# Performance work log

Measured on AMD Instinct MI355X. Metric: run time of the kernel, lower is better.

The kernel has to match this reference:

```python
import jax, jax.numpy as jnp
import numpy as np

K, D = 2048, 256
B, H, W = 16, 64, 64
DECAY = 0.99
EPS = 1e-05


def setup_inputs() -> dict:
    key = jax.random.key(0)
    k1, k2, k3 = jax.random.split(key, 3)
    z_e = jax.random.normal(k1, (B, D, H, W), dtype=jnp.float32)
    codebook = jax.random.normal(k2, (K, D), dtype=jnp.float32)
    ema_count = jnp.zeros((K,), dtype=jnp.float32)
    ema_weight = jax.random.normal(k3, (K, D), dtype=jnp.float32)
    return {"z_e": z_e, "codebook": codebook, "ema_count": ema_count, "ema_weight": ema_weight}


def reference(z_e, codebook, ema_count, ema_weight):
    b, d, h, w = z_e.shape
    k = codebook.shape[0]
    # [B, D, H, W] -> [B*H*W, D]
    flat = jnp.transpose(z_e, (0, 2, 3, 1)).reshape(-1, d)
    # squared euclidean distances to each code: [N, K]
    dist = (jnp.sum(flat * flat, axis=1, keepdims=True)
            - 2.0 * (flat @ codebook.T)
            + jnp.sum(codebook * codebook, axis=1))
    idx = jnp.argmin(dist, axis=1)  # [N] int
    # gather nearest codes -> [B, D, H, W]
    z_q = jnp.transpose(codebook[idx].reshape(b, h, w, d), (0, 3, 1, 2))
    # EMA statistics (training path, no_grad in torch)
    n = jax.ops.segment_sum(jnp.ones_like(idx, dtype=flat.dtype), idx, num_segments=k)  # [K]
    dw = jax.ops.segment_sum(flat, idx, num_segments=k)  # [K, D]
    new_ema_count = ema_count * DECAY + (1.0 - DECAY) * n
    new_ema_weight = ema_weight * DECAY + (1.0 - DECAY) * dw
    new_codebook = new_ema_weight / (new_ema_count + EPS)[:, None]
    # commitment loss and straight-through estimator
    loss_commit = jnp.mean(jnp.square(z_e - z_q))
    z_q_st = z_e + jax.lax.stop_gradient(z_q - z_e)
    return (z_q_st, idx.reshape(b, h, w), loss_commit,
            new_codebook, new_ema_count, new_ema_weight)
```

## Files before the change

kernel.cpp:

```cpp
#include <hip/hip_runtime.h>
#include <hip/hip_bf16.h>


#define KC 2048
#define DD 256
#define NB 16
#define HWS 4096
#define NPTS 65536
#define DECAYF 0.99f
#define ONEMD 0.01f
#define EPSF 1e-5f
#define NCH 2
#define MARGIN 0.0625f
#define CHPTS 32
#define FPT 64
#define NLOSS 4096

typedef __attribute__((ext_vector_type(8))) short short8v;
typedef __attribute__((ext_vector_type(16))) float f32x16;

#define WS_IDX     0
#define WS_SORTED  262144
#define WS_CNTI    524288
#define WS_START   532480
#define WS_CURSOR  540672
#define WS_FLAGCNT 548864
#define WS_FLAGS   549120
#define WS_LOSSP   549120
#define WS_CNORM   811264
#define WS_PART    819456
#define WS_CBH     5013760
#define WS_CBL     6062336
#define WS_ZH      7110912
#define WS_ZL      40665344
#define WS_NEED_MFMA 74219776ULL
#define WS_NEED_MID  5013760ULL

#define OUT_ZQ   0
#define OUT_IDX  16777216
#define OUT_LOSS (OUT_IDX + NPTS)
#define OUT_CB   (OUT_LOSS + 1)
#define OUT_CNT  (OUT_CB + KC*DD)
#define OUT_W    (OUT_CNT + KC)

static __device__ __forceinline__ unsigned short f2bf_rn(float x) {
    unsigned u = __builtin_bit_cast(unsigned, x);
    unsigned r = (u + 0x7FFFu + ((u >> 16) & 1u)) >> 16;
    return (unsigned short)r;
}
static __device__ __forceinline__ float bf2f(unsigned short h) {
    unsigned u = ((unsigned)h) << 16;
    return __builtin_bit_cast(float, u);
}
static __device__ __forceinline__ void gload_lds16(const unsigned short* g,
                                                   unsigned short* l) {
    __builtin_amdgcn_global_load_lds(
        (const __attribute__((address_space(1))) void*)g,
        (__attribute__((address_space(3))) void*)l, 16, 0, 0);
}

__global__ __launch_bounds__(256) void prep_kernel(const float* __restrict__ z_e,
                                                   const float* __restrict__ cb,
                                                   float* __restrict__ cnorm,
                                                   unsigned short* __restrict__ cbs_h,
                                                   unsigned short* __restrict__ cbs_l,
                                                   unsigned short* __restrict__ zh,
                                                   unsigned short* __restrict__ zl,
                                                   int* __restrict__ cnti,
                                                   int* __restrict__ flagcnt) {
    const int tid = threadIdx.x;
    if (blockIdx.x >= 4096) {
        int k = (blockIdx.x - 4096) * 256 + tid;
        cnti[k] = 0;
        if (k == 0) *flagcnt = 0;
        const int ct = k >> 5, lc = k & 31;
        const float4* row = reinterpret_cast<const float4*>(cb + (size_t)k * DD);
        float s = 0.f;
        #pragma unroll 4
        for (int chunk = 0; chunk < 32; ++chunk) {
            float4 v0 = row[chunk * 2], v1 = row[chunk * 2 + 1];
            float v[8] = {v0.x, v0.y, v0.z, v0.w, v1.x, v1.y, v1.z, v1.w};
            unsigned short hh[8], ll[8];
            #pragma unroll
            for (int j = 0; j < 8; ++j) {
                s += v[j] * v[j];
                hh[j] = f2bf_rn(v[j]);
                ll[j] = f2bf_rn(v[j] - bf2f(hh[j]));
            }
            const int ks = chunk >> 1, h = chunk & 1;
            size_t dst = (size_t)ct * 8192 + ks * 512 + (h * 32 + lc) * 8;
            *reinterpret_cast<ushort4*>(cbs_h + dst)     = *(ushort4*)&hh[0];
            *reinterpret_cast<ushort4*>(cbs_h + dst + 4) = *(ushort4*)&hh[4];
            *reinterpret_cast<ushort4*>(cbs_l + dst)     = *(ushort4*)&ll[0];
            *reinterpret_cast<ushort4*>(cbs_l + dst + 4) = *(ushort4*)&ll[4];
        }
        cnorm[k] = s;
        return;
    }
    __shared__ float t_lds[64][65];
    const int bid = blockIdx.x;
    const int hw0 = (bid & 63) * 64;
    const int d0 = ((bid >> 6) & 3) * 64;
    const int b = bid >> 8;
    const float* src = z_e + (size_t)b * DD * HWS;
    #pragma unroll
    for (int i = 0; i < 16; ++i) {
        int li = tid + i * 256;
        int d = li >> 6, hw = li & 63;
        t_lds[d][hw] = src[(size_t)(d0 + d) * HWS + hw0 + hw];
    }
    __syncthreads();
    #pragma unroll
    for (int i = 0; i < 16; ++i) {
        int li = tid + i * 256;
        int p = li >> 6, d = li & 63;
        float x = t_lds[d][p];
        unsigned short h = f2bf_rn(x);
        unsigned short l = f2bf_rn(x - bf2f(h));
        size_t o = ((size_t)b * HWS + hw0 + p) * DD + d0 + d;
        zh[o] = h; zl[o] = l;
    }
}

__global__ __launch_bounds__(256) void cnorm_kernel(const float* __restrict__ cb,
                                                    float* __restrict__ cnorm) {
    int k = blockIdx.x * 256 + threadIdx.x;
    if (k < KC) {
        const float4* row = reinterpret_cast<const float4*>(cb + (size_t)k * DD);
        float s = 0.f;
        #pragma unroll 8
        for (int i = 0; i < DD / 4; ++i) {
            float4 v = row[i];
            s += v.x * v.x + v.y * v.y + v.z * v.z + v.w * v.w;
        }
        cnorm[k] = s;
    }
}

__global__ __launch_bounds__(256, 2) void argmin_mfma_kernel(const unsigned short* __restrict__ zh,
                                                             const unsigned short* __restrict__ zl,
                                                             const unsigned short* __restrict__ cbs_h,
                                                             const unsigned short* __restrict__ cbs_l,
                                                             const float* __restrict__ cnorm,
                                                             int* __restrict__ idx_out,
                                                             int* __restrict__ cnti,
                                                             int* __restrict__ flagcnt,
                                                             int* __restrict__ flaglist,
                                                             unsigned long long* __restrict__ fixmin) {
    __shared__ unsigned short lds_cb[2][2][16][512];

    const int tid = threadIdx.x;
    const int w = tid >> 6, lane = tid & 63;
    const int lc = lane & 31, h = lane >> 5;
    const int p = blockIdx.x * 128 + w * 32 + lc;

    const short8v* zhp = reinterpret_cast<const short8v*>(zh + (size_t)p * DD + h * 8);
    const short8v* zlp = reinterpret_cast<const short8v*>(zl + (size_t)p * DD + h * 8);
    short8v bh[16], bl[16];
    #pragma unroll
    for (int ks = 0; ks < 16; ++ks) { bh[ks] = zhp[ks * 2]; bl[ks] = zlp[ks * 2]; }

    auto stage = [&](int ct, int buf) {
        #pragma unroll
        for (int j = 0; j < 8; ++j) {
            const int inst = w * 8 + j;
            const int part = inst >> 4;
            const int ks = inst & 15;
            const unsigned short* src =
                (part ? cbs_l : cbs_h) + (size_t)ct * 8192 + ks * 512 + lane * 8;
            gload_lds16(src, &lds_cb[buf][part][ks][0]);
        }
    };

    float bv1 = 3.4e38f, bv2 = 3.4e38f;
    int bi1 = 0;
    int cur = 0;

    stage(0, 0);
    __syncthreads();

    for (int ct = 0; ct < KC / 32; ++ct) {
        if (ct + 1 < KC / 32) stage(ct + 1, cur ^ 1);

        f32x16 a0, a1, a2;
        #pragma unroll
        for (int i = 0; i < 16; ++i) { a0[i] = 0.f; a1[i] = 0.f; a2[i] = 0.f; }
        #pragma unroll
        for (int ks = 0; ks < 16; ++ks) {
            short8v ah = *reinterpret_cast<const short8v*>(&lds_cb[cur][0][ks][lane * 8]);
            short8v al = *reinterpret_cast<const short8v*>(&lds_cb[cur][1][ks][lane * 8]);
            a0 = __builtin_amdgcn_mfma_f32_32x32x16_bf16(ah, bh[ks], a0, 0, 0, 0);
            a1 = __builtin_amdgcn_mfma_f32_32x32x16_bf16(ah, bl[ks], a1, 0, 0, 0);
            a2 = __builtin_amdgcn_mfma_f32_32x32x16_bf16(al, bh[ks], a2, 0, 0, 0);
        }
        const float* cnb = cnorm + ct * 32 + h * 4;
        #pragma unroll
        for (int g = 0; g < 4; ++g) {
            float4 cn = *reinterpret_cast<const float4*>(cnb + g * 8);
            float cna[4] = {cn.x, cn.y, cn.z, cn.w};
            #pragma unroll
            for (int q = 0; q < 4; ++q) {
                float dot = a0[g * 4 + q] + a1[g * 4 + q] + a2[g * 4 + q];
                float v = fmaf(dot, -2.0f, cna[q]);
                int k = ct * 32 + g * 8 + h * 4 + q;
                bool lt = v < bv1;
                bv2 = fminf(bv2, fmaxf(v, bv1));
                bv1 = fminf(bv1, v);
                bi1 = lt ? k : bi1;
            }
        }
        __syncthreads();
        cur ^= 1;
    }

    float ov1 = __shfl_xor(bv1, 32, 64);
    float ov2 = __shfl_xor(bv2, 32, 64);
    int   oi1 = __shfl_xor(bi1, 32, 64);
    float nv1 = fminf(bv1, ov1);
    float nv2 = fminf(fmaxf(bv1, ov1), fminf(bv2, ov2));
    int ni1 = (ov1 < bv1 || (ov1 == bv1 && oi1 < bi1)) ? oi1 : bi1;

    if (h == 0) {
        idx_out[p] = ni1;
        atomicAdd(&cnti[ni1], 1);
        if (nv2 - nv1 < MARGIN) {
            int pos = atomicAdd(flagcnt, 1);
            flaglist[pos] = p;
            fixmin[pos] = ~0ULL;
        }
    }
}

__global__ __launch_bounds__(256) void fixup_part_kernel(const float* __restrict__ z_e,
                                                         const float* __restrict__ cb,
                                                         const float* __restrict__ cnorm,
                                                         const int* __restrict__ flagcnt,
                                                         const int* __restrict__ flaglist,
                                                         unsigned long long* __restrict__ fixmin) {
    __shared__ float As[64][FPT + 4];
    __shared__ float Bs[64][64 + 4];
    __shared__ float rv[FPT][16];
    __shared__ int   ri[FPT][16];
    __shared__ int   zo[FPT];

    const int tid = threadIdx.x;
    const int tx = tid & 15, ty = tid >> 4;
    const int tot = *flagcnt;
    const int base = blockIdx.x * FPT;
    if (base >= tot) return;
    const int cnt = min(FPT, tot - base);
    const int kt = blockIdx.y * 64;

    if (tid < FPT) {
        int n = flaglist[base + ((tid < cnt) ? tid : 0)];
        zo[tid] = (n >> 12) * DD * HWS + (n & 4095);
    }
    __syncthreads();

    float acc[4][4] = {};
    for (int dc = 0; dc < DD; dc += 64) {
        #pragma unroll
        for (int i = 0; i < 16; ++i) {
            int li = tid + i * 256;
            int d = li >> 6, pp = li & 63;
            As[d][pp] = z_e[(size_t)zo[pp] + (size_t)(dc + d) * HWS];
        }
        #pragma unroll
        for (int i = 0; i < 16; ++i) {
            int li = tid + i * 256;
            int k = li >> 6, d = li & 63;
            Bs[d][k] = cb[(size_t)(kt + k) * DD + dc + d];
        }
        __syncthreads();
        #pragma unroll
        for (int d = 0; d < 64; ++d) {
            const float4 a4 = *reinterpret_cast<const float4*>(&As[d][ty * 4]);
            const float4 b4 = *reinterpret_cast<const float4*>(&Bs[d][tx * 4]);
            const float a[4] = {a4.x, a4.y, a4.z, a4.w};
            const float bb[4] = {b4.x, b4.y, b4.z, b4.w};
            #pragma unroll
            for (int j = 0; j < 4; ++j)
                #pragma unroll
                for (int i = 0; i < 4; ++i)
                    acc[j][i] = fmaf(a[j], bb[i], acc[j][i]);
        }
        __syncthreads();
    }

    float bestv[4]; int besti[4];
    #pragma unroll
    for (int j = 0; j < 4; ++j) { bestv[j] = 3.4e38f; besti[j] = 0; }
    #pragma unroll
    for (int i = 0; i < 4; ++i) {
        int k = kt + tx * 4 + i;
        float c = cnorm[k];
        #pragma unroll
        for (int j = 0; j < 4; ++j) {
            float dist = c - 2.0f * acc[j][i];
            if (dist < bestv[j]) { bestv[j] = dist; besti[j] = k; }
        }
    }
    #pragma unroll
    for (int j = 0; j < 4; ++j) { rv[ty * 4 + j][tx] = bestv[j]; ri[ty * 4 + j][tx] = besti[j]; }
    __syncthreads();

    if (tid < cnt) {
        float bv = rv[tid][0]; int bi = ri[tid][0];
        #pragma unroll
        for (int t = 1; t < 16; ++t) {
            float v = rv[tid][t]; int i2 = ri[tid][t];
            if (v < bv || (v == bv && i2 < bi)) { bv = v; bi = i2; }
        }
        unsigned uv = __float_as_uint(bv);
        uv = (uv & 0x80000000u) ? ~uv : (uv | 0x80000000u);
        unsigned long long key = ((unsigned long long)uv << 32) | (unsigned)bi;
        atomicMin(&fixmin[base + tid], key);
    }
}

__global__ __launch_bounds__(256) void fixup_apply_kernel(const int* __restrict__ flagcnt,
                                                          const int* __restrict__ flaglist,
                                                          const unsigned long long* __restrict__ fixmin,
                                                          int* __restrict__ idx_out,
                                                          int* __restrict__ cnti) {
    int f = blockIdx.x * 256 + threadIdx.x;
    if (f < *flagcnt) {
        int n = flaglist[f];
        int nk = (int)(fixmin[f] & 0xFFFFFFFFull);
        int ok = idx_out[n];
        if (nk != ok) {
            atomicSub(&cnti[ok], 1);
            atomicAdd(&cnti[nk], 1);
            idx_out[n] = nk;
        }
    }
}

#define PT 64
#define KT 64
#define DC 64
__global__ __launch_bounds__(256) void argmin_kernel(const float* __restrict__ z_e,
                                                     const float* __restrict__ cb,
                                                     const float* __restrict__ cnorm,
                                                     int* __restrict__ idx_out) {
    __shared__ float As[DC][PT + 4];
    __shared__ float Bs[DC][KT + 4];
    __shared__ float rv[PT][16];
    __shared__ int   ri[PT][16];
    const int tid = threadIdx.x;
    const int tx = tid & 15, ty = tid >> 4;
    const int n0 = blockIdx.x * PT;
    const int b = n0 >> 12;
    const int hw0 = n0 & 4095;
    const float* zb = z_e + (size_t)b * DD * HWS + hw0;
    float bestv[4]; int besti[4];
    #pragma unroll
    for (int j = 0; j < 4; ++j) { bestv[j] = 3.4e38f; besti[j] = 0; }
    for (int kt = 0; kt < KC; kt += KT) {
        float acc[4][4] = {};
        for (int dc = 0; dc < DD; dc += DC) {
            #pragma unroll
            for (int i = 0; i < 16; ++i) {
                int li = tid + i * 256;
                int d = li >> 6, pp = li & 63;
                As[d][pp] = zb[(size_t)(dc + d) * HWS + pp];
            }
            #pragma unroll
            for (int i = 0; i < 16; ++i) {
                int li = tid + i * 256;
                int k = li >> 6, d = li & 63;
                Bs[d][k] = cb[(size_t)(kt + k) * DD + dc + d];
            }
            __syncthreads();
            #pragma unroll
            for (int d = 0; d < DC; ++d) {
                const float4 a4 = *reinterpret_cast<const float4*>(&As[d][ty * 4]);
                const float4 b4 = *reinterpret_cast<const float4*>(&Bs[d][tx * 4]);
                const float a[4] = {a4.x, a4.y, a4.z, a4.w};
                const float bb[4] = {b4.x, b4.y, b4.z, b4.w};
                #pragma unroll
                for (int j = 0; j < 4; ++j)
                    #pragma unroll
                    for (int i = 0; i < 4; ++i)
                        acc[j][i] = fmaf(a[j], bb[i], acc[j][i]);
            }
            __syncthreads();
        }
        #pragma unroll
        for (int i = 0; i < 4; ++i) {
            int k = kt + tx * 4 + i;
            float c = cnorm[k];
            #pragma unroll
            for (int j = 0; j < 4; ++j) {
                float dist = c - 2.0f * acc[j][i];
                if (dist < bestv[j]) { bestv[j] = dist; besti[j] = k; }
            }
        }
    }
    #pragma unroll
    for (int j = 0; j < 4; ++j) { rv[ty * 4 + j][tx] = bestv[j]; ri[ty * 4 + j][tx] = besti[j]; }
    __syncthreads();
    if (tid < PT) {
        float bv = rv[tid][0]; int bi = ri[tid][0];
        #pragma unroll
        for (int t = 1; t < 16; ++t) {
            float v = rv[tid][t]; int i2 = ri[tid][t];
            if (v < bv || (v == bv && i2 < bi)) { bv = v; bi = i2; }
        }
        idx_out[n0 + tid] = bi;
    }
}

__global__ __launch_bounds__(256) void hist_kernel(const int* __restrict__ idx,
                                                   int* __restrict__ cnti) {
    int n = blockIdx.x * 256 + threadIdx.x;
    atomicAdd(&cnti[idx[n]], 1);
}

__global__ __launch_bounds__(256) void scan_kernel(const int* __restrict__ cnt,
                                                   int* __restrict__ start,
                                                   int* __restrict__ cursor) {
    __shared__ int ps[256];
    const int t = threadIdx.x;
    int v[8], s = 0;
    #pragma unroll
    for (int j = 0; j < 8; ++j) { v[j] = cnt[t * 8 + j]; s += v[j]; }
    ps[t] = s;
    __syncthreads();
    for (int off = 1; off < 256; off <<= 1) {
        int x = (t >= off) ? ps[t - off] : 0;
        __syncthreads();
        ps[t] += x;
        __syncthreads();
    }
    int base = ps[t] - s;
    #pragma unroll
    for (int j = 0; j < 8; ++j) { start[t * 8 + j] = base; cursor[t * 8 + j] = base; base += v[j]; }
}

__global__ __launch_bounds__(256) void scatter_ids_kernel(const int* __restrict__ idx,
                                                          int* __restrict__ cursor,
                                                          int* __restrict__ sorted,
                                                          float* __restrict__ out_idxf,
                                                          float* __restrict__ dwacc) {
    int n = blockIdx.x * 256 + threadIdx.x;
    int k = idx[n];
    out_idxf[n] = (float)k;
    int pos = atomicAdd(&cursor[k], 1);
    sorted[pos] = n;
    #pragma unroll
    for (int i = 0; i < (KC * DD) / NPTS; ++i)
        dwacc[n + i * NPTS] = 0.f;
}

__global__ __launch_bounds__(256) void dw_chunk_kernel(const unsigned short* __restrict__ zh,
                                                       const unsigned short* __restrict__ zl,
                                                       const int* __restrict__ sorted,
                                                       const int* __restrict__ idx,
                                                       float* __restrict__ dwacc) {
    const int t = threadIdx.x;
    const int base = blockIdx.x * CHPTS;
    int kcur = idx[sorted[base]];
    float acc = 0.f;
    for (int i = 0; i < CHPTS; ++i) {
        const int n = sorted[base + i];
        const int k = idx[n];
        if (k != kcur) {
            atomicAdd(&dwacc[(size_t)kcur * DD + t], acc);
            acc = 0.f; kcur = k;
        }
        acc += bf2f(zh[(size_t)n * DD + t]) + bf2f(zl[(size_t)n * DD + t]);
    }
    atomicAdd(&dwacc[(size_t)kcur * DD + t], acc);
}

__global__ __launch_bounds__(256) void dw_direct_kernel(const float* __restrict__ z_e,
                                                        const int* __restrict__ sorted,
                                                        const int* __restrict__ start,
                                                        const int* __restrict__ cnti,
                                                        float* __restrict__ part) {
    const int k = blockIdx.x, c = blockIdx.y, t = threadIdx.x;
    const int s0 = start[k], cnt = cnti[k];
    float acc = 0.f;
    for (int p = c; p < cnt; p += NCH) {
        int n = sorted[s0 + p];
        int b = n >> 12, hw = n & 4095;
        acc += z_e[(size_t)b * DD * HWS + (size_t)t * HWS + hw];
    }
    part[((size_t)k * NCH + c) * DD + t] = acc;
}

__global__ __launch_bounds__(256) void zq_loss_kernel(const float* __restrict__ z_e,
                                                      const float* __restrict__ cb,
                                                      const int* __restrict__ idx,
                                                      float* __restrict__ out_zq,
                                                      float* __restrict__ lossp) {
    const int tid = threadIdx.x;
    const size_t base = ((size_t)blockIdx.x * 256 + tid) * 16;
    const int hw = (int)(base & 4095);
    const int d = (int)((base >> 12) & 255);
    const int b = (int)(base >> 20);
    const int n0 = b * HWS + hw;

    const int4* ip = reinterpret_cast<const int4*>(idx + n0);
    const float4* zp = reinterpret_cast<const float4*>(z_e + base);
    float4* op = reinterpret_cast<float4*>(out_zq + base);

    float ls = 0.f;
    #pragma unroll
    for (int g = 0; g < 4; ++g) {
        int4 i4 = ip[g];
        float4 z4 = zp[g];
        int kk[4] = {i4.x, i4.y, i4.z, i4.w};
        float zz[4] = {z4.x, z4.y, z4.z, z4.w};
        float o4[4];
        #pragma unroll
        for (int q = 0; q < 4; ++q) {
            float qv = cb[(size_t)kk[q] * DD + d];
            o4[q] = zz[q] + (qv - zz[q]);
            float df = zz[q] - qv;
            ls += df * df;
        }
        float4 w4; w4.x = o4[0]; w4.y = o4[1]; w4.z = o4[2]; w4.w = o4[3];
        op[g] = w4;
    }

    #pragma unroll
    for (int off = 32; off > 0; off >>= 1) ls += __shfl_down(ls, off, 64);
    __shared__ float wsum[4];
    if ((tid & 63) == 0) wsum[tid >> 6] = ls;
    __syncthreads();
    if (tid == 0) lossp[blockIdx.x] = wsum[0] + wsum[1] + wsum[2] + wsum[3];
}

__global__ __launch_bounds__(256) void finalize_dw_kernel(const float* __restrict__ ema_count,
                                                          const float* __restrict__ ema_weight,
                                                          const int* __restrict__ cnti,
                                                          const float* __restrict__ dwacc,
                                                          const float* __restrict__ lossp,
                                                          float* __restrict__ out_cb,
                                                          float* __restrict__ out_cnt,
                                                          float* __restrict__ out_w,
                                                          float* __restrict__ out_loss) {
    const int t = blockIdx.x * 256 + threadIdx.x;
    const int k = t >> 8, d = t & 255;
    const float nc = ema_count[k] * DECAYF + ONEMD * (float)cnti[k];
    const float nw = ema_weight[t] * DECAYF + ONEMD * dwacc[t];
    out_w[t] = nw;
    out_cb[t] = nw / (nc + EPSF);
    if (d == 0) out_cnt[k] = nc;

    if (blockIdx.x == 0) {
        __shared__ double sd[256];
        const int tid = threadIdx.x;
        double s = 0.0;
        for (int i = tid; i < NLOSS; i += 256) s += (double)lossp[i];
        sd[tid] = s;
        __syncthreads();
        for (int off = 128; off > 0; off >>= 1) {
            if (tid < off) sd[tid] += sd[tid + off];
            __syncthreads();
        }
        if (tid == 0) out_loss[0] = (float)(sd[0] / 16777216.0);
    }
}

__global__ __launch_bounds__(256) void finalize_part_kernel(const float* __restrict__ ema_count,
                                                            const float* __restrict__ ema_weight,
                                                            const int* __restrict__ cnti,
                                                            const float* __restrict__ part,
                                                            const float* __restrict__ lossp,
                                                            float* __restrict__ out_cb,
                                                            float* __restrict__ out_cnt,
                                                            float* __restrict__ out_w,
                                                            float* __restrict__ out_loss) {
    const int t = blockIdx.x * 256 + threadIdx.x;
    const int k = t >> 8, d = t & 255;
    float dw = 0.f;
    #pragma unroll
    for (int c = 0; c < NCH; ++c) dw += part[((size_t)k * NCH + c) * DD + d];
    const float nc = ema_count[k] * DECAYF + ONEMD * (float)cnti[k];
    const float nw = ema_weight[t] * DECAYF + ONEMD * dw;
    out_w[t] = nw;
    out_cb[t] = nw / (nc + EPSF);
    if (d == 0) out_cnt[k] = nc;

    if (blockIdx.x == 0) {
        __shared__ double sd[256];
        const int tid = threadIdx.x;
        double s = 0.0;
        for (int i = tid; i < NLOSS; i += 256) s += (double)lossp[i];
        sd[tid] = s;
        __syncthreads();
        for (int off = 128; off > 0; off >>= 1) {
            if (tid < off) sd[tid] += sd[tid + off];
            __syncthreads();
        }
        if (tid == 0) out_loss[0] = (float)(sd[0] / 16777216.0);
    }
}

extern "C" void kernel_launch(void* const* d_in, const int* in_sizes, int n_in,
                              void* d_out, int out_size, void* d_ws, size_t ws_size,
                              hipStream_t stream) {
    const float* z_e       = (const float*)d_in[0];
    const float* codebook  = (const float*)d_in[1];
    const float* ema_count = (const float*)d_in[2];
    const float* ema_weight= (const float*)d_in[3];
    float* out = (float*)d_out;
    char* ws = (char*)d_ws;

    int*   ws_idx    = (int*)(ws + WS_IDX);
    int*   ws_sorted = (int*)(ws + WS_SORTED);
    int*   ws_cnti   = (int*)(ws + WS_CNTI);
    int*   ws_start  = (int*)(ws + WS_START);
    int*   ws_cursor = (int*)(ws + WS_CURSOR);
    int*   ws_flagc  = (int*)(ws + WS_FLAGCNT);
    int*   ws_flags  = (int*)(ws + WS_FLAGS);
    float* ws_lossp  = (float*)(ws + WS_LOSSP);
    float* ws_cnorm  = (float*)(ws + WS_CNORM);
    unsigned long long* ws_fixmin = (unsigned long long*)(ws + WS_PART);
    float* ws_dwacc  = (float*)(ws + WS_PART);
    float* ws_part   = (float*)(ws + WS_PART);
    unsigned short* ws_cbh = (unsigned short*)(ws + WS_CBH);
    unsigned short* ws_cbl = (unsigned short*)(ws + WS_CBL);
    unsigned short* ws_zh  = (unsigned short*)(ws + WS_ZH);
    unsigned short* ws_zl  = (unsigned short*)(ws + WS_ZL);

    const bool mfma_path = (ws_size >= WS_NEED_MFMA);
    const bool mid_path  = (ws_size >= WS_NEED_MID);

    if (mfma_path) {
        prep_kernel<<<4104, 256, 0, stream>>>(z_e, codebook, ws_cnorm, ws_cbh, ws_cbl,
                                              ws_zh, ws_zl, ws_cnti, ws_flagc);
        argmin_mfma_kernel<<<NPTS / 128, 256, 0, stream>>>(ws_zh, ws_zl, ws_cbh, ws_cbl,
                                                           ws_cnorm, ws_idx, ws_cnti,
                                                           ws_flagc, ws_flags, ws_fixmin);
        fixup_part_kernel<<<dim3(NPTS / FPT, KC / 64), 256, 0, stream>>>(z_e, codebook, ws_cnorm,
                                                                         ws_flagc, ws_flags,
                                                                         ws_fixmin);
        fixup_apply_kernel<<<NPTS / 256, 256, 0, stream>>>(ws_flagc, ws_flags, ws_fixmin,
                                                           ws_idx, ws_cnti);
        zq_loss_kernel<<<NLOSS, 256, 0, stream>>>(z_e, codebook, ws_idx,
                                                  out + OUT_ZQ, ws_lossp);
        scan_kernel<<<1, 256, 0, stream>>>(ws_cnti, ws_start, ws_cursor);
        scatter_ids_kernel<<<NPTS / 256, 256, 0, stream>>>(ws_idx, ws_cursor, ws_sorted,
                                                           out + OUT_IDX, ws_dwacc);
        dw_chunk_kernel<<<NPTS / CHPTS, 256, 0, stream>>>(ws_zh, ws_zl, ws_sorted,
                                                          ws_idx, ws_dwacc);
        finalize_dw_kernel<<<(KC * DD) / 256, 256, 0, stream>>>(ema_count, ema_weight,
                                                                ws_cnti, ws_dwacc, ws_lossp,
                                                                out + OUT_CB, out + OUT_CNT,
                                                                out + OUT_W, out + OUT_LOSS);
    } else if (mid_path) {
        hipMemsetAsync(ws + WS_CNTI, 0, (size_t)(WS_FLAGCNT + 256 - WS_CNTI), stream);
        cnorm_kernel<<<(KC + 255) / 256, 256, 0, stream>>>(codebook, ws_cnorm);
        argmin_kernel<<<NPTS / PT, 256, 0, stream>>>(z_e, codebook, ws_cnorm, ws_idx);
        zq_loss_kernel<<<NLOSS, 256, 0, stream>>>(z_e, codebook, ws_idx,
                                                  out + OUT_ZQ, ws_lossp);
        hist_kernel<<<NPTS / 256, 256, 0, stream>>>(ws_idx, ws_cnti);
        scan_kernel<<<1, 256, 0, stream>>>(ws_cnti, ws_start, ws_cursor);
        scatter_ids_kernel<<<NPTS / 256, 256, 0, stream>>>(ws_idx, ws_cursor, ws_sorted,
                                                           out + OUT_IDX, ws_part);
        dw_direct_kernel<<<dim3(KC, NCH), 256, 0, stream>>>(z_e, ws_sorted,
                                                            ws_start, ws_cnti, ws_part + KC * DD);
        finalize_part_kernel<<<(KC * DD) / 256, 256, 0, stream>>>(ema_count, ema_weight,
                                                                  ws_cnti, ws_part + KC * DD,
                                                                  ws_lossp,
                                                                  out + OUT_CB, out + OUT_CNT,
                                                                  out + OUT_W, out + OUT_LOSS);
    }
}
```

Measured before the change: 409.3 us.

## Double per-wave point tile in MFMA argmin and fuse tail kernels

```diff
diff --git a/kernel.cpp b/kernel.cpp
--- a/kernel.cpp
+++ b/kernel.cpp
@@ -137,7 +137,7 @@
     }
 }
 
-__global__ __launch_bounds__(256, 2) void argmin_mfma_kernel(const unsigned short* __restrict__ zh,
+__global__ __launch_bounds__(256, 1) void argmin_mfma_kernel(const unsigned short* __restrict__ zh,
                                                              const unsigned short* __restrict__ zl,
                                                              const unsigned short* __restrict__ cbs_h,
                                                              const unsigned short* __restrict__ cbs_l,
@@ -152,13 +152,19 @@
     const int tid = threadIdx.x;
     const int w = tid >> 6, lane = tid & 63;
     const int lc = lane & 31, h = lane >> 5;
-    const int p = blockIdx.x * 128 + w * 32 + lc;
-
-    const short8v* zhp = reinterpret_cast<const short8v*>(zh + (size_t)p * DD + h * 8);
-    const short8v* zlp = reinterpret_cast<const short8v*>(zl + (size_t)p * DD + h * 8);
-    short8v bh[16], bl[16];
-    #pragma unroll
-    for (int ks = 0; ks < 16; ++ks) { bh[ks] = zhp[ks * 2]; bl[ks] = zlp[ks * 2]; }
+    const int p0 = blockIdx.x * 256 + w * 64 + lc;
+    const int p1 = p0 + 32;
+
+    const short8v* zhp0 = reinterpret_cast<const short8v*>(zh + (size_t)p0 * DD + h * 8);
+    const short8v* zlp0 = reinterpret_cast<const short8v*>(zl + (size_t)p0 * DD + h * 8);
+    const short8v* zhp1 = reinterpret_cast<const short8v*>(zh + (size_t)p1 * DD + h * 8);
+    const short8v* zlp1 = reinterpret_cast<const short8v*>(zl + (size_t)p1 * DD + h * 8);
+    short8v bh0[16], bl0[16], bh1[16], bl1[16];
+    #pragma unroll
+    for (int ks = 0; ks < 16; ++ks) {
+        bh0[ks] = zhp0[ks * 2]; bl0[ks] = zlp0[ks * 2];
+        bh1[ks] = zhp1[ks * 2]; bl1[ks] = zlp1[ks * 2];
+    }
 
     auto stage = [&](int ct, int buf) {
         #pragma unroll
@@ -172,8 +178,9 @@
         }
     };
 
-    float bv1 = 3.4e38f, bv2 = 3.4e38f;
-    int bi1 = 0;
+    float bv1_0 = 3.4e38f, bv2_0 = 3.4e38f;
+    float bv1_1 = 3.4e38f, bv2_1 = 3.4e38f;
+    int bi1_0 = 0, bi1_1 = 0;
     int cur = 0;
 
     stage(0, 0);
@@ -182,16 +189,22 @@
     for (int ct = 0; ct < KC / 32; ++ct) {
         if (ct + 1 < KC / 32) stage(ct + 1, cur ^ 1);
 
-        f32x16 a0, a1, a2;
-        #pragma unroll
-        for (int i = 0; i < 16; ++i) { a0[i] = 0.f; a1[i] = 0.f; a2[i] = 0.f; }
+        f32x16 a0, a1, a2, c0, c1, c2;
+        #pragma unroll
+        for (int i = 0; i < 16; ++i) {
+            a0[i] = 0.f; a1[i] = 0.f; a2[i] = 0.f;
+            c0[i] = 0.f; c1[i] = 0.f; c2[i] = 0.f;
+        }
         #pragma unroll
         for (int ks = 0; ks < 16; ++ks) {
             short8v ah = *reinterpret_cast<const short8v*>(&lds_cb[cur][0][ks][lane * 8]);
             short8v al = *reinterpret_cast<const short8v*>(&lds_cb[cur][1][ks][lane * 8]);
-            a0 = __builtin_amdgcn_mfma_f32_32x32x16_bf16(ah, bh[ks], a0, 0, 0, 0);
-            a1 = __builtin_amdgcn_mfma_f32_32x32x16_bf16(ah, bl[ks], a1, 0, 0, 0);
-            a2 = __builtin_amdgcn_mfma_f32_32x32x16_bf16(al, bh[ks], a2, 0, 0, 0);
+            a0 = __builtin_amdgcn_mfma_f32_32x32x16_bf16(ah, bh0[ks], a0, 0, 0, 0);
+            c0 = __builtin_amdgcn_mfma_f32_32x32x16_bf16(ah, bh1[ks], c0, 0, 0, 0);
+            a1 = __builtin_amdgcn_mfma_f32_32x32x16_bf16(ah, bl0[ks], a1, 0, 0, 0);
+            c1 = __builtin_amdgcn_mfma_f32_32x32x16_bf16(ah, bl1[ks], c1, 0, 0, 0);
+            a2 = __builtin_amdgcn_mfma_f32_32x32x16_bf16(al, bh0[ks], a2, 0, 0, 0);
+            c2 = __builtin_amdgcn_mfma_f32_32x32x16_bf16(al, bh1[ks], c2, 0, 0, 0);
         }
         const float* cnb = cnorm + ct * 32 + h * 4;
         #pragma unroll
@@ -200,33 +213,57 @@
             float cna[4] = {cn.x, cn.y, cn.z, cn.w};
             #pragma unroll
             for (int q = 0; q < 4; ++q) {
-                float dot = a0[g * 4 + q] + a1[g * 4 + q] + a2[g * 4 + q];
-                float v = fmaf(dot, -2.0f, cna[q]);
                 int k = ct * 32 + g * 8 + h * 4 + q;
-                bool lt = v < bv1;
-                bv2 = fminf(bv2, fmaxf(v, bv1));
-                bv1 = fminf(bv1, v);
-                bi1 = lt ? k : bi1;
+                float dot0 = a0[g * 4 + q] + a1[g * 4 + q] + a2[g * 4 + q];
+                float v0 = fmaf(dot0, -2.0f, cna[q]);
+                bool lt0 = v0 < bv1_0;
+                bv2_0 = fminf(bv2_0, fmaxf(v0, bv1_0));
+                bv1_0 = fminf(bv1_0, v0);
+                bi1_0 = lt0 ? k : bi1_0;
+                float dot1 = c0[g * 4 + q] + c1[g * 4 + q] + c2[g * 4 + q];
+                float v1 = fmaf(dot1, -2.0f, cna[q]);
+                bool lt1 = v1 < bv1_1;
+                bv2_1 = fminf(bv2_1, fmaxf(v1, bv1_1));
+                bv1_1 = fminf(bv1_1, v1);
+                bi1_1 = lt1 ? k : bi1_1;
             }
         }
         __syncthreads();
         cur ^= 1;
     }
 
-    float ov1 = __shfl_xor(bv1, 32, 64);
-    float ov2 = __shfl_xor(bv2, 32, 64);
-    int   oi1 = __shfl_xor(bi1, 32, 64);
-    float nv1 = fminf(bv1, ov1);
-    float nv2 = fminf(fmaxf(bv1, ov1), fminf(bv2, ov2));
-    int ni1 = (ov1 < bv1 || (ov1 == bv1 && oi1 < bi1)) ? oi1 : bi1;
-
-    if (h == 0) {
-        idx_out[p] = ni1;
-        atomicAdd(&cnti[ni1], 1);
-        if (nv2 - nv1 < MARGIN) {
-            int pos = atomicAdd(flagcnt, 1);
-            flaglist[pos] = p;
-            fixmin[pos] = ~0ULL;
+    {
+        float ov1 = __shfl_xor(bv1_0, 32, 64);
+        float ov2 = __shfl_xor(bv2_0, 32, 64);
+        int   oi1 = __shfl_xor(bi1_0, 32, 64);
+        float nv1 = fminf(bv1_0, ov1);
+        float nv2 = fminf(fmaxf(bv1_0, ov1), fminf(bv2_0, ov2));
+        int ni1 = (ov1 < bv1_0 || (ov1 == bv1_0 && oi1 < bi1_0)) ? oi1 : bi1_0;
+        if (h == 0) {
+            idx_out[p0] = ni1;
+            atomicAdd(&cnti[ni1], 1);
+            if (nv2 - nv1 < MARGIN) {
+                int pos = atomicAdd(flagcnt, 1);
+                flaglist[pos] = p0;
+                fixmin[pos] = ~0ULL;
+            }
+        }
+    }
+    {
+        float ov1 = __shfl_xor(bv1_1, 32, 64);
+        float ov2 = __shfl_xor(bv2_1, 32, 64);
+        int   oi1 = __shfl_xor(bi1_1, 32, 64);
+        float nv1 = fminf(bv1_1, ov1);
+        float nv2 = fminf(fmaxf(bv1_1, ov1), fminf(bv2_1, ov2));
+        int ni1 = (ov1 < bv1_1 || (ov1 == bv1_1 && oi1 < bi1_1)) ? oi1 : bi1_1;
+        if (h == 0) {
+            idx_out[p1] = ni1;
+            atomicAdd(&cnti[ni1], 1);
+            if (nv2 - nv1 < MARGIN) {
+                int pos = atomicAdd(flagcnt, 1);
+                flaglist[pos] = p1;
+                fixmin[pos] = ~0ULL;
+            }
         }
     }
 }
@@ -246,85 +283,90 @@
     const int tid = threadIdx.x;
     const int tx = tid & 15, ty = tid >> 4;
     const int tot = *flagcnt;
-    const int base = blockIdx.x * FPT;
-    if (base >= tot) return;
-    const int cnt = min(FPT, tot - base);
     const int kt = blockIdx.y * 64;
 
-    if (tid < FPT) {
-        int n = flaglist[base + ((tid < cnt) ? tid : 0)];
-        zo[tid] = (n >> 12) * DD * HWS + (n & 4095);
-    }
-    __syncthreads();
-
-    float acc[4][4] = {};
-    for (int dc = 0; dc < DD; dc += 64) {
-        #pragma unroll
-        for (int i = 0; i < 16; ++i) {
-            int li = tid + i * 256;
-            int d = li >> 6, pp = li & 63;
-            As[d][pp] = z_e[(size_t)zo[pp] + (size_t)(dc + d) * HWS];
-        }
-        #pragma unroll
-        for (int i = 0; i < 16; ++i) {
-            int li = tid + i * 256;
-            int k = li >> 6, d = li & 63;
-            Bs[d][k] = cb[(size_t)(kt + k) * DD + dc + d];
-        }
+    for (int cbk = blockIdx.x; cbk * FPT < tot; cbk += gridDim.x) {
+        const int base = cbk * FPT;
+        const int cnt = min(FPT, tot - base);
         __syncthreads();
-        #pragma unroll
-        for (int d = 0; d < 64; ++d) {
-            const float4 a4 = *reinterpret_cast<const float4*>(&As[d][ty * 4]);
-            const float4 b4 = *reinterpret_cast<const float4*>(&Bs[d][tx * 4]);
-            const float a[4] = {a4.x, a4.y, a4.z, a4.w};
-            const float bb[4] = {b4.x, b4.y, b4.z, b4.w};
-            #pragma unroll
-            for (int j = 0; j < 4; ++j)
+        if (tid < FPT) {
+            int n = flaglist[base + ((tid < cnt) ? tid : 0)];
+            zo[tid] = (n >> 12) * DD * HWS + (n & 4095);
+        }
+        __syncthreads();
+
+        float acc[4][4] = {};
+        for (int dc = 0; dc < DD; dc += 64) {
+            #pragma unroll
+            for (int i = 0; i < 16; ++i) {
+                int li = tid + i * 256;
+                int d = li >> 6, pp = li & 63;
+                As[d][pp] = z_e[(size_t)zo[pp] + (size_t)(dc + d) * HWS];
+            }
+            #pragma unroll
+            for (int i = 0; i < 16; ++i) {
+                int li = tid + i * 256;
+                int k = li >> 6, d = li & 63;
+                Bs[d][k] = cb[(size_t)(kt + k) * DD + dc + d];
+            }
+            __syncthreads();
+            #pragma unroll
+            for (int d = 0; d < 64; ++d) {
+                const float4 a4 = *reinterpret_cast<const float4*>(&As[d][ty * 4]);
+                const float4 b4 = *reinterpret_cast<const float4*>(&Bs[d][tx * 4]);
+                const float a[4] = {a4.x, a4.y, a4.z, a4.w};
+                const float bb[4] = {b4.x, b4.y, b4.z, b4.w};
                 #pragma unroll
-                for (int i = 0; i < 4; ++i)
-                    acc[j][i] = fmaf(a[j], bb[i], acc[j][i]);
-        }
+                for (int j = 0; j < 4; ++j)
+                    #pragma unroll
+                    for (int i = 0; i < 4; ++i)
+                        acc[j][i] = fmaf(a[j], bb[i], acc[j][i]);
+            }
+            __syncthreads();
+        }
+
+        float bestv[4]; int besti[4];
+        #pragma unroll
+        for (int j = 0; j < 4; ++j) { bestv[j] = 3.4e38f; besti[j] = 0; }
+        #pragma unroll
+        for (int i = 0; i < 4; ++i) {
+            int k = kt + tx * 4 + i;
+            float c = cnorm[k];
+            #pragma unroll
+            for (int j = 0; j < 4; ++j) {
+                float dist = c - 2.0f * acc[j][i];
+                if (dist < bestv[j]) { bestv[j] = dist; besti[j] = k; }
+            }
+        }
+        #pragma unroll
+        for (int j = 0; j < 4; ++j) { rv[ty * 4 + j][tx] = bestv[j]; ri[ty * 4 + j][tx] = besti[j]; }
         __syncthreads();
-    }
-
-    float bestv[4]; int besti[4];
-    #pragma unroll
-    for (int j = 0; j < 4; ++j) { bestv[j] = 3.4e38f; besti[j] = 0; }
-    #pragma unroll
-    for (int i = 0; i < 4; ++i) {
-        int k = kt + tx * 4 + i;
-        float c = cnorm[k];
-        #pragma unroll
-        for (int j = 0; j < 4; ++j) {
-            float dist = c - 2.0f * acc[j][i];
-            if (dist < bestv[j]) { bestv[j] = dist; besti[j] = k; }
-        }
-    }
-    #pragma unroll
-    for (int j = 0; j < 4; ++j) { rv[ty * 4 + j][tx] = bestv[j]; ri[ty * 4 + j][tx] = besti[j]; }
-    __syncthreads();
-
-    if (tid < cnt) {
-        float bv = rv[tid][0]; int bi = ri[tid][0];
-        #pragma unroll
-        for (int t = 1; t < 16; ++t) {
-            float v = rv[tid][t]; int i2 = ri[tid][t];
-            if (v < bv || (v == bv && i2 < bi)) { bv = v; bi = i2; }
-        }
-        unsigned uv = __float_as_uint(bv);
-        uv = (uv & 0x80000000u) ? ~uv : (uv | 0x80000000u);
-        unsigned long long key = ((unsigned long long)uv << 32) | (unsigned)bi;
-        atomicMin(&fixmin[base + tid], key);
-    }
-}
-
-__global__ __launch_bounds__(256) void fixup_apply_kernel(const int* __restrict__ flagcnt,
-                                                          const int* __restrict__ flaglist,
-                                                          const unsigned long long* __restrict__ fixmin,
-                                                          int* __restrict__ idx_out,
-                                                          int* __restrict__ cnti) {
-    int f = blockIdx.x * 256 + threadIdx.x;
-    if (f < *flagcnt) {
+
+        if (tid < cnt) {
+            float bv = rv[tid][0]; int bi = ri[tid][0];
+            #pragma unroll
+            for (int t = 1; t < 16; ++t) {
+                float v = rv[tid][t]; int i2 = ri[tid][t];
+                if (v < bv || (v == bv && i2 < bi)) { bv = v; bi = i2; }
+            }
+            unsigned uv = __float_as_uint(bv);
+            uv = (uv & 0x80000000u) ? ~uv : (uv | 0x80000000u);
+            unsigned long long key = ((unsigned long long)uv << 32) | (unsigned)bi;
+            atomicMin(&fixmin[base + tid], key);
+        }
+    }
+}
+
+__global__ __launch_bounds__(256) void scan_apply_kernel(const int* __restrict__ flagcnt,
+                                                         const int* __restrict__ flaglist,
+                                                         const unsigned long long* __restrict__ fixmin,
+                                                         int* __restrict__ idx_out,
+                                                         int* __restrict__ cnti,
+                                                         int* __restrict__ start,
+                                                         int* __restrict__ cursor) {
+    const int t = threadIdx.x;
+    const int tot = *flagcnt;
+    for (int f = t; f < tot; f += 256) {
         int n = flaglist[f];
         int nk = (int)(fixmin[f] & 0xFFFFFFFFull);
         int ok = idx_out[n];
@@ -334,6 +376,23 @@
             idx_out[n] = nk;
         }
     }
+    __syncthreads();
+
+    __shared__ int ps[256];
+    int v[8], s = 0;
+    #pragma unroll
+    for (int j = 0; j < 8; ++j) { v[j] = cnti[t * 8 + j]; s += v[j]; }
+    ps[t] = s;
+    __syncthreads();
+    for (int off = 1; off < 256; off <<= 1) {
+        int x = (t >= off) ? ps[t - off] : 0;
+        __syncthreads();
+        ps[t] += x;
+        __syncthreads();
+    }
+    int base = ps[t] - s;
+    #pragma unroll
+    for (int j = 0; j < 8; ++j) { start[t * 8 + j] = base; cursor[t * 8 + j] = base; base += v[j]; }
 }
 
 #define PT 64
@@ -417,40 +476,15 @@
     atomicAdd(&cnti[idx[n]], 1);
 }
 
-__global__ __launch_bounds__(256) void scan_kernel(const int* __restrict__ cnt,
-                                                   int* __restrict__ start,
-                                                   int* __restrict__ cursor) {
-    __shared__ int ps[256];
-    const int t = threadIdx.x;
-    int v[8], s = 0;
-    #pragma unroll
-    for (int j = 0; j < 8; ++j) { v[j] = cnt[t * 8 + j]; s += v[j]; }
-    ps[t] = s;
-    __syncthreads();
-    for (int off = 1; off < 256; off <<= 1) {
-        int x = (t >= off) ? ps[t - off] : 0;
-        __syncthreads();
-        ps[t] += x;
-        __syncthreads();
-    }
-    int base = ps[t] - s;
-    #pragma unroll
-    for (int j = 0; j < 8; ++j) { start[t * 8 + j] = base; cursor[t * 8 + j] = base; base += v[j]; }
-}
-
 __global__ __launch_bounds__(256) void scatter_ids_kernel(const int* __restrict__ idx,
                                                           int* __restrict__ cursor,
                                                           int* __restrict__ sorted,
-                                                          float* __restrict__ out_idxf,
-                                                          float* __restrict__ dwacc) {
+                                                          float* __restrict__ out_idxf) {
     int n = blockIdx.x * 256 + threadIdx.x;
     int k = idx[n];
     out_idxf[n] = (float)k;
     int pos = atomicAdd(&cursor[k], 1);
     sorted[pos] = n;
-    #pragma unroll
-    for (int i = 0; i < (KC * DD) / NPTS; ++i)
-        dwacc[n + i * NPTS] = 0.f;
 }
 
 __global__ __launch_bounds__(256) void dw_chunk_kernel(const unsigned short* __restrict__ zh,
@@ -490,11 +524,16 @@
     part[((size_t)k * NCH + c) * DD + t] = acc;
 }
 
-__global__ __launch_bounds__(256) void zq_loss_kernel(const float* __restrict__ z_e,
-                                                      const float* __restrict__ cb,
-                                                      const int* __restrict__ idx,
-                                                      float* __restrict__ out_zq,
-                                                      float* __restrict__ lossp) {
+__global__ __launch_bounds__(256) void zq_scatter_kernel(const float* __restrict__ z_e,
+                                                         const float* __restrict__ cb,
+                                                         const int* __restrict__ idx,
+                                                         float* __restrict__ out_zq,
+                                                         float* __restrict__ lossp,
+                                                         int* __restrict__ cursor,
+                                                         int* __restrict__ sorted,
+                                                         float* __restrict__ out_idxf,
+                                                         float* __restrict__ dwacc,
+                                                         int fuse_tail) {
     const int tid = threadIdx.x;
     const size_t base = ((size_t)blockIdx.x * 256 + tid) * 16;
     const int hw = (int)(base & 4095);
@@ -531,6 +570,17 @@
     if ((tid & 63) == 0) wsum[tid >> 6] = ls;
     __syncthreads();
     if (tid == 0) lossp[blockIdx.x] = wsum[0] + wsum[1] + wsum[2] + wsum[3];
+
+    if (fuse_tail && blockIdx.x < 256) {
+        int n = blockIdx.x * 256 + tid;
+        int k = idx[n];
+        out_idxf[n] = (float)k;
+        int pos = atomicAdd(&cursor[k], 1);
+        sorted[pos] = n;
+        #pragma unroll
+        for (int i = 0; i < (KC * DD) / NPTS; ++i)
+            dwacc[n + i * NPTS] = 0.f;
+    }
 }
 
 __global__ __launch_bounds__(256) void finalize_dw_kernel(const float* __restrict__ ema_count,
@@ -633,19 +683,18 @@
     if (mfma_path) {
         prep_kernel<<<4104, 256, 0, stream>>>(z_e, codebook, ws_cnorm, ws_cbh, ws_cbl,
                                               ws_zh, ws_zl, ws_cnti, ws_flagc);
-        argmin_mfma_kernel<<<NPTS / 128, 256, 0, stream>>>(ws_zh, ws_zl, ws_cbh, ws_cbl,
+        argmin_mfma_kernel<<<NPTS / 256, 256, 0, stream>>>(ws_zh, ws_zl, ws_cbh, ws_cbl,
                                                            ws_cnorm, ws_idx, ws_cnti,
                                                            ws_flagc, ws_flags, ws_fixmin);
-        fixup_part_kernel<<<dim3(NPTS / FPT, KC / 64), 256, 0, stream>>>(z_e, codebook, ws_cnorm,
-                                                                         ws_flagc, ws_flags,
-                                                                         ws_fixmin);
-        fixup_apply_kernel<<<NPTS / 256, 256, 0, stream>>>(ws_flagc, ws_flags, ws_fixmin,
-                                                           ws_idx, ws_cnti);
-        zq_loss_kernel<<<NLOSS, 256, 0, stream>>>(z_e, codebook, ws_idx,
-                                                  out + OUT_ZQ, ws_lossp);
-        scan_kernel<<<1, 256, 0, stream>>>(ws_cnti, ws_start, ws_cursor);
-        scatter_ids_kernel<<<NPTS / 256, 256, 0, stream>>>(ws_idx, ws_cursor, ws_sorted,
-                                                           out + OUT_IDX, ws_dwacc);
+        fixup_part_kernel<<<dim3(128, KC / 64), 256, 0, stream>>>(z_e, codebook, ws_cnorm,
+                                                                  ws_flagc, ws_flags,
+                                                                  ws_fixmin);
+        scan_apply_kernel<<<1, 256, 0, stream>>>(ws_flagc, ws_flags, ws_fixmin,
+                                                 ws_idx, ws_cnti, ws_start, ws_cursor);
+        zq_scatter_kernel<<<NLOSS, 256, 0, stream>>>(z_e, codebook, ws_idx,
+                                                     out + OUT_ZQ, ws_lossp,
+                                                     ws_cursor, ws_sorted,
+                                                     out + OUT_IDX, ws_dwacc, 1);
         dw_chunk_kernel<<<NPTS / CHPTS, 256, 0, stream>>>(ws_zh, ws_zl, ws_sorted,
                                                           ws_idx, ws_dwacc);
         finalize_dw_kernel<<<(KC * DD) / 256, 256, 0, stream>>>(ema_count, ema_weight,
@@ -656,12 +705,15 @@
         hipMemsetAsync(ws + WS_CNTI, 0, (size_t)(WS_FLAGCNT + 256 - WS_CNTI), stream);
         cnorm_kernel<<<(KC + 255) / 256, 256, 0, stream>>>(codebook, ws_cnorm);
         argmin_kernel<<<NPTS / PT, 256, 0, stream>>>(z_e, codebook, ws_cnorm, ws_idx);
-        zq_loss_kernel<<<NLOSS, 256, 0, stream>>>(z_e, codebook, ws_idx,
-                                                  out + OUT_ZQ, ws_lossp);
         hist_kernel<<<NPTS / 256, 256, 0, stream>>>(ws_idx, ws_cnti);
-        scan_kernel<<<1, 256, 0, stream>>>(ws_cnti, ws_start, ws_cursor);
+        scan_apply_kernel<<<1, 256, 0, stream>>>(ws_flagc, ws_flags, ws_fixmin,
+                                                 ws_idx, ws_cnti, ws_start, ws_cursor);
+        zq_scatter_kernel<<<NLOSS, 256, 0, stream>>>(z_e, codebook, ws_idx,
+                                                     out + OUT_ZQ, ws_lossp,
+                                                     ws_cursor, ws_sorted,
+                                                     out + OUT_IDX, ws_part, 0);
         scatter_ids_kernel<<<NPTS / 256, 256, 0, stream>>>(ws_idx, ws_cursor, ws_sorted,
-                                                           out + OUT_IDX, ws_part);
+                                                           out + OUT_IDX);
         dw_direct_kernel<<<dim3(KC, NCH), 256, 0, stream>>>(z_e, ws_sorted,
                                                             ws_start, ws_cnti, ws_part + KC * DD);
         finalize_part_kernel<<<(KC * DD) / 256, 256, 0, stream>>>(ema_count, ema_weight,
```

New measurement: 416.3 us. Within noise of the previous version (+1.7%).
